# Kernel optimization log

Hardware: AMD Instinct MI355X
Metric: run time of the kernel (lower is better)

## Reference

```python
import jax, jax.numpy as jnp
import numpy as np

N_HEADS = 16
ROPE_BASE = 10000.0


def _rope_cos_sin(seq_len, head_dim, dtype):
    half = head_dim // 2
    inv_freq = 1.0 / (ROPE_BASE ** (jnp.arange(0, half, dtype=jnp.float32) / half))
    ang = jnp.arange(seq_len, dtype=jnp.float32)[:, None] * inv_freq[None, :]  # [S, half]
    cos = jnp.concatenate([jnp.cos(ang), jnp.cos(ang)], axis=-1).astype(dtype)  # [S, hd]
    sin = jnp.concatenate([jnp.sin(ang), jnp.sin(ang)], axis=-1).astype(dtype)
    return cos, sin


def _rotate_half(x):
    half = x.shape[-1] // 2
    return jnp.concatenate([-x[..., half:], x[..., :half]], axis=-1)


def setup_inputs() -> dict:
    key = jax.random.key(0)
    k1, k2, k3 = jax.random.split(key, 3)
    B, S, D = 2, 2048, 1024
    x = jax.random.normal(k1, (B, S, D), dtype=jnp.float32)
    w_qkv = jax.random.normal(k2, (D, 3 * D), dtype=jnp.float32) * (1.0 / np.sqrt(D))
    w_out = jax.random.normal(k3, (D, D), dtype=jnp.float32) * (1.0 / np.sqrt(D))
    return {"x": x, "w_qkv": w_qkv, "w_out": w_out}


def reference(x, w_qkv, w_out):
    B, S, D = x.shape
    H = N_HEADS
    hd = D // H
    scale = 1.0 / np.sqrt(hd)

    qkv = x @ w_qkv  # [B, S, 3D]
    q, k, v = jnp.split(qkv, 3, axis=-1)
    # [B, H, S, hd]
    q = q.reshape(B, S, H, hd).transpose(0, 2, 1, 3)
    k = k.reshape(B, S, H, hd).transpose(0, 2, 1, 3)
    v = v.reshape(B, S, H, hd).transpose(0, 2, 1, 3)

    cos, sin = _rope_cos_sin(S, hd, x.dtype)  # [S, hd]
    q = q * cos + _rotate_half(q) * sin
    k = k * cos + _rotate_half(k) * sin

    scores = jnp.einsum("bhqd,bhkd->bhqk", q, k) * scale  # [B, H, S, S]
    causal = jnp.tril(jnp.ones((S, S), dtype=bool))
    scores = jnp.where(causal[None, None, :, :], scores, -jnp.inf)

    probs = jax.nn.softmax(scores.astype(jnp.float32), axis=-1).astype(q.dtype)
    out = jnp.einsum("bhqk,bhkd->bhqd", probs, v)  # [B, H, S, hd]
    out = out.transpose(0, 2, 1, 3).reshape(B, S, D)
    return out @ w_out
```

## Files before the change

kernel.cpp:

```cpp
#include <hip/hip_runtime.h>
#include <math.h>
#include <type_traits>

#define B_  2
#define S_  2048
#define D_  1024
#define H_  16

typedef short bf16x8 __attribute__((ext_vector_type(8)));
typedef short bf16x4 __attribute__((ext_vector_type(4)));
typedef float f32x4  __attribute__((ext_vector_type(4)));

__device__ __forceinline__ short f2bf(float f) {
    unsigned u = __builtin_bit_cast(unsigned, f);
    u += 0x7FFFu + ((u >> 16) & 1u);
    return (short)(u >> 16);
}
__device__ __forceinline__ float bf2f(short s) {
    unsigned u = ((unsigned)(unsigned short)s) << 16;
    return __builtin_bit_cast(float, u);
}

__device__ __forceinline__ void gload16(const short* g, const void* l) {
    __builtin_amdgcn_global_load_lds(
        (const __attribute__((address_space(1))) void*)g,
        (__attribute__((address_space(3))) void*)l, 16, 0, 0);
}

__global__ __launch_bounds__(256) void cvt_bf16_kernel(
    const float* __restrict__ in, short* __restrict__ out)
{
    int i = (blockIdx.x * 256 + threadIdx.x) * 8;
    float4 a = *(const float4*)(in + i);
    float4 b = *(const float4*)(in + i + 4);
    bf16x8 o;
    o[0] = f2bf(a.x); o[1] = f2bf(a.y); o[2] = f2bf(a.z); o[3] = f2bf(a.w);
    o[4] = f2bf(b.x); o[5] = f2bf(b.y); o[6] = f2bf(b.z); o[7] = f2bf(b.w);
    *(bf16x8*)(out + i) = o;
}

__global__ __launch_bounds__(256) void transpose_cvt_kernel(
    const float* __restrict__ in, short* __restrict__ out, int K, int N)
{
    __shared__ short t[64][72];
    const int k0 = blockIdx.y * 64, n0 = blockIdx.x * 64;
    const int r = threadIdx.x >> 2;
    const int c = (threadIdx.x & 3) * 16;
    const float* src = in + (size_t)(k0 + r) * N + n0 + c;
#pragma unroll
    for (int i = 0; i < 16; ++i) t[c + i][r] = f2bf(src[i]);
    __syncthreads();
    short* dst = out + (size_t)(n0 + r) * K + k0 + c;
    *(bf16x8*)(dst)     = *(const bf16x8*)&t[r][c];
    *(bf16x8*)(dst + 8) = *(const bf16x8*)&t[r][c + 8];
}

__global__ __launch_bounds__(256) void rope_tab_kernel(float2* __restrict__ tab)
{
    int idx = blockIdx.x * 256 + threadIdx.x;
    int j = idx & 31, s = idx >> 5;
    float inv = powf(10000.0f, -(float)j * (1.0f / 32.0f));
    float sn, cs;
    sincosf((float)s * inv, &sn, &cs);
    tab[idx] = make_float2(cs, sn);
}

__global__ __launch_bounds__(256) void gemm_bt_f32(
    const short* __restrict__ A, const short* __restrict__ Bt,
    float* __restrict__ C, int M, int N, int K)
{
    __shared__ short smem[18432];

    const int tid  = threadIdx.x;
    const int wave = tid >> 6, lane = tid & 63;
    const int quad = lane >> 4, l16 = lane & 15;
    const int wm = wave >> 1, wn = wave & 1;
    const int row0 = blockIdx.y * 128, col0 = blockIdx.x * 64;

    f32x4 acc[4][2];
#pragma unroll
    for (int mi = 0; mi < 4; ++mi)
#pragma unroll
        for (int ni = 0; ni < 2; ++ni) acc[mi][ni] = (f32x4)0.f;

    const int sr = tid >> 2;
    const int sc = (tid & 3) * 8;
    const short* a0 = A  + (size_t)(row0 + sr) * K + sc;
    const short* a1 = A  + (size_t)(row0 + 64 + sr) * K + sc;
    const short* b0 = Bt + (size_t)(col0 + sr) * K + sc;

    auto stage = [&](int b, int kt) {
        char* l = (char*)(smem + b * 6144) + wave * 1024;
        const int k0 = kt * 32;
        gload16(a0 + k0, l);
        gload16(a1 + k0, l + 4096);
        gload16(b0 + k0, l + 8192);
    };

    const int NT = K >> 5;
    stage(0, 0);
    stage(1, 1);
    int bufid = 0;
    for (int kt = 0; kt < NT; ++kt) {
        if (kt + 1 < NT) { asm volatile("s_waitcnt vmcnt(3)" ::: "memory"); }
        else             { asm volatile("s_waitcnt vmcnt(0)" ::: "memory"); }
        __builtin_amdgcn_s_barrier();
        __builtin_amdgcn_sched_barrier(0);
        if (kt + 2 < NT) {
            int nb = bufid + 2; if (nb >= 3) nb -= 3;
            stage(nb, kt + 2);
        }

        const short* As = smem + bufid * 6144;
        const short* Bs = As + 4096;
        bf16x8 af[4], bfr[2];
#pragma unroll
        for (int mi = 0; mi < 4; ++mi)
            af[mi] = *(const bf16x8*)(As + (wm * 64 + mi * 16 + l16) * 32 + quad * 8);
#pragma unroll
        for (int ni = 0; ni < 2; ++ni)
            bfr[ni] = *(const bf16x8*)(Bs + (wn * 32 + ni * 16 + l16) * 32 + quad * 8);
#pragma unroll
        for (int mi = 0; mi < 4; ++mi)
#pragma unroll
            for (int ni = 0; ni < 2; ++ni)
                acc[mi][ni] = __builtin_amdgcn_mfma_f32_16x16x32_bf16(
                    af[mi], bfr[ni], acc[mi][ni], 0, 0, 0);

        bufid = (bufid + 1 == 3) ? 0 : bufid + 1;
    }

#pragma unroll
    for (int mi = 0; mi < 4; ++mi)
#pragma unroll
        for (int ni = 0; ni < 2; ++ni)
#pragma unroll
            for (int r = 0; r < 4; ++r) {
                int row = row0 + wm * 64 + mi * 16 + quad * 4 + r;
                int col = col0 + wn * 32 + ni * 16 + l16;
                C[(size_t)row * N + col] = acc[mi][ni][r];
            }
}

__global__ __launch_bounds__(256) void gemm_qkv(
    const short* __restrict__ A, const short* __restrict__ Bt,
    const float2* __restrict__ tab,
    short* __restrict__ Qb, short* __restrict__ Kb, short* __restrict__ Vt)
{
    const int K = 1024;
    extern __shared__ short smem[];
    short* Sc = smem;

    const int tid  = threadIdx.x;
    const int wave = tid >> 6, lane = tid & 63;
    const int quad = lane >> 4, l16 = lane & 15;
    const int wm = wave >> 1, wn = wave & 1;
    const int row0 = blockIdx.y * 128, col0 = blockIdx.x * 128;

    f32x4 acc[4][4];
#pragma unroll
    for (int mi = 0; mi < 4; ++mi)
#pragma unroll
        for (int ni = 0; ni < 4; ++ni) acc[mi][ni] = (f32x4)0.f;

    const int sr = tid >> 2;
    const int sc = (tid & 3) * 8;
    const short* a0 = A  + (size_t)(row0 + sr) * K + sc;
    const short* a1 = A  + (size_t)(row0 + 64 + sr) * K + sc;
    const short* b0 = Bt + (size_t)(col0 + sr) * K + sc;
    const short* b1 = Bt + (size_t)(col0 + 64 + sr) * K + sc;

    auto stage = [&](int b, int kt) {
        char* l = (char*)(smem + b * 8192) + wave * 1024;
        const int k0 = kt * 32;
        gload16(a0 + k0, l);
        gload16(a1 + k0, l + 4096);
        gload16(b0 + k0, l + 8192);
        gload16(b1 + k0, l + 12288);
    };

    const int NT = K >> 5;
    stage(0, 0);
    stage(1, 1);
    int bufid = 0;
    for (int kt = 0; kt < NT; ++kt) {
        if (kt + 1 < NT) { asm volatile("s_waitcnt vmcnt(4)" ::: "memory"); }
        else             { asm volatile("s_waitcnt vmcnt(0)" ::: "memory"); }
        __builtin_amdgcn_s_barrier();
        __builtin_amdgcn_sched_barrier(0);
        if (kt + 2 < NT) {
            int nb = bufid + 2; if (nb >= 3) nb -= 3;
            stage(nb, kt + 2);
        }

        const short* As = smem + bufid * 8192;
        const short* Bs = As + 4096;
        bf16x8 af[4], bfr[4];
#pragma unroll
        for (int mi = 0; mi < 4; ++mi)
            af[mi] = *(const bf16x8*)(As + (wm * 64 + mi * 16 + l16) * 32 + quad * 8);
#pragma unroll
        for (int ni = 0; ni < 4; ++ni)
            bfr[ni] = *(const bf16x8*)(Bs + (wn * 64 + ni * 16 + l16) * 32 + quad * 8);
#pragma unroll
        for (int mi = 0; mi < 4; ++mi)
#pragma unroll
            for (int ni = 0; ni < 4; ++ni)
                acc[mi][ni] = __builtin_amdgcn_mfma_f32_16x16x32_bf16(
                    af[mi], bfr[ni], acc[mi][ni], 0, 0, 0);

        bufid = (bufid + 1 == 3) ? 0 : bufid + 1;
    }

    __syncthreads();

    const int sec  = (col0 + wn * 64) >> 6;
    const int h    = sec & 15;
    const int kind = sec >> 4;
    short* myS = Sc + wave * 4608;

    const int mrow0 = row0 + wm * 64;
    const int b  = mrow0 >> 11;
    const int bh = b * 16 + h;
    const int sbase = mrow0 & (S_ - 1);

    if (kind < 2) {
#pragma unroll
        for (int mi = 0; mi < 4; ++mi) {
#pragma unroll
            for (int r = 0; r < 4; ++r) {
                int sl = mi * 16 + quad * 4 + r;
                int s = sbase + sl;
#pragma unroll
                for (int ni = 0; ni < 2; ++ni) {
                    int j = ni * 16 + l16;
                    float2 t = tab[s * 32 + j];
                    float lo = acc[mi][ni][r], hi = acc[mi][ni + 2][r];
                    float olo = lo * t.x - hi * t.y;
                    float ohi = hi * t.x + lo * t.y;
                    if (kind == 0) { olo *= 0.125f; ohi *= 0.125f; }
                    myS[sl * 72 + j]      = f2bf(olo);
                    myS[sl * 72 + 32 + j] = f2bf(ohi);
                }
            }
        }
        const int rl = lane >> 3;
        const int cl = (lane & 7) * 8;
        short* dst = (kind == 0 ? Qb : Kb);
#pragma unroll
        for (int p = 0; p < 8; ++p) {
            int rr = p * 8 + rl;
            bf16x8 v = *(const bf16x8*)&myS[rr * 72 + cl];
            *(bf16x8*)(dst + ((size_t)bh * S_ + sbase + rr) * 64 + cl) = v;
        }
    } else {
#pragma unroll
        for (int mi = 0; mi < 4; ++mi)
#pragma unroll
            for (int ni = 0; ni < 4; ++ni) {
                bf16x4 p;
                p[0] = f2bf(acc[mi][ni][0]);
                p[1] = f2bf(acc[mi][ni][1]);
                p[2] = f2bf(acc[mi][ni][2]);
                p[3] = f2bf(acc[mi][ni][3]);
                *(bf16x4*)&myS[(ni * 16 + l16) * 72 + mi * 16 + quad * 4] = p;
            }
        const int rl = lane >> 3;
        const int cl = (lane & 7) * 8;
#pragma unroll
        for (int p = 0; p < 8; ++p) {
            int dd = p * 8 + rl;
            bf16x8 v = *(const bf16x8*)&myS[dd * 72 + cl];
            *(bf16x8*)(Vt + ((size_t)bh * 64 + dd) * S_ + sbase + cl) = v;
        }
    }
}

__global__ __launch_bounds__(256, 3) void attn_kernel(
    const short* __restrict__ Qb, const short* __restrict__ Kb,
    const short* __restrict__ Vt, short* __restrict__ Opart,
    float* __restrict__ lpart)
{
    __shared__ short Ks[2][64 * 64];
    __shared__ short Vs[2][64 * 64];
    __shared__ short Ps[128][72];

    const int lin = blockIdx.x;
    const int xcd = lin & 7;
    const int j   = lin >> 3;
    const int bh   = xcd * 4 + (j & 3);
    const int task = j >> 2;

    const int g = task < 4 ? 0 : task < 12 ? 1 : task < 24 ? 2 : 3;
    const int cumstart = g == 0 ? 0 : g == 1 ? 4 : g == 2 ? 12 : 24;
    const int idx = task - cumstart;
    const int qd = idx / (g + 1);
    const int qb = 4 * g + qd;
    const int c  = idx - qd * (g + 1);
    const int t0 = c * 8;
    const int t1 = min(2 * qb + 1, c * 8 + 7);

    const int wave = threadIdx.x >> 6, lane = threadIdx.x & 63;
    const int quad = lane >> 4, l16 = lane & 15;
    const int subr  = lane >> 3;
    const int chunk = (lane & 7) ^ subr;
    const size_t head64 = (size_t)bh * S_ * 64;

    bf16x8 qf[2][2];
#pragma unroll
    for (int m = 0; m < 2; ++m) {
        const short* qrow = Qb + head64
            + (size_t)(qb * 128 + wave * 32 + m * 16 + l16) * 64 + quad * 8;
        qf[m][0] = *(const bf16x8*)(qrow);
        qf[m][1] = *(const bf16x8*)(qrow + 32);
    }

    bf16x8 ones;
#pragma unroll
    for (int i = 0; i < 8; ++i) ones[i] = (short)0x3F80;

    auto stage = [&](int buf, int t) {
        const short* kt = Kb + head64 + (size_t)(t * 64 + wave * 16) * 64;
        const short* vt = Vt + head64 + (size_t)(wave * 16) * S_ + t * 64;
        char* kl = (char*)(Ks[buf]) + wave * 2048;
        char* vl = (char*)(Vs[buf]) + wave * 2048;
#pragma unroll
        for (int g2 = 0; g2 < 2; ++g2) {
            gload16(kt + (g2 * 8 + subr) * 64 + chunk * 8, kl + g2 * 1024);
            gload16(vt + (size_t)(g2 * 8 + subr) * S_ + chunk * 8, vl + g2 * 1024);
        }
    };

    f32x4 lacc[2] = {(f32x4)0.f, (f32x4)0.f};
    f32x4 oacc[2][4];
#pragma unroll
    for (int m = 0; m < 2; ++m)
#pragma unroll
        for (int nt = 0; nt < 4; ++nt) oacc[m][nt] = (f32x4)0.f;

    stage(0, t0);
    int buf = 0;
    for (int t = t0; t <= t1; ++t) {
        __builtin_amdgcn_s_barrier();
        if (t < t1) stage(buf ^ 1, t + 1);
        if (t < t1) { asm volatile("s_waitcnt vmcnt(4)" ::: "memory"); }
        else        { asm volatile("s_waitcnt vmcnt(0)" ::: "memory"); }
        __builtin_amdgcn_s_barrier();
        __builtin_amdgcn_sched_barrier(0);

        const short* kbuf = Ks[buf];
        const short* vbuf = Vs[buf];

        f32x4 s4[2][4];
#pragma unroll
        for (int nt = 0; nt < 4; ++nt) {
            const int krow = nt * 16 + l16;
            const int sw = krow & 7;
            bf16x8 k0 = *(const bf16x8*)(kbuf + krow * 64 + ((quad ^ sw) << 3));
            bf16x8 k1 = *(const bf16x8*)(kbuf + krow * 64 + (((quad + 4) ^ sw) << 3));
#pragma unroll
            for (int m = 0; m < 2; ++m) {
                f32x4 a = (f32x4)0.f;
                a = __builtin_amdgcn_mfma_f32_16x16x32_bf16(k0, qf[m][0], a, 0, 0, 0);
                a = __builtin_amdgcn_mfma_f32_16x16x32_bf16(k1, qf[m][1], a, 0, 0, 0);
                s4[m][nt] = a;
            }
        }

        if (t >= 2 * qb) {
            const int kbase = (t - 2 * qb) * 64;
#pragma unroll
            for (int m = 0; m < 2; ++m) {
                const int qq = wave * 32 + m * 16 + l16;
#pragma unroll
                for (int nt = 0; nt < 4; ++nt)
#pragma unroll
                    for (int r = 0; r < 4; ++r)
                        if (kbase + nt * 16 + quad * 4 + r > qq)
                            s4[m][nt][r] = -INFINITY;
            }
        }

#pragma unroll
        for (int m = 0; m < 2; ++m)
#pragma unroll
            for (int nt = 0; nt < 4; ++nt) {
                bf16x4 p;
#pragma unroll
                for (int r = 0; r < 4; ++r)
                    p[r] = f2bf(__expf(s4[m][nt][r] - 8.0f));
                *(bf16x4*)&Ps[wave * 32 + m * 16 + l16][nt * 16 + quad * 4] = p;
            }

        bf16x8 pa[2][2];
#pragma unroll
        for (int m = 0; m < 2; ++m) {
            pa[m][0] = *(const bf16x8*)&Ps[wave * 32 + m * 16 + l16][quad * 8];
            pa[m][1] = *(const bf16x8*)&Ps[wave * 32 + m * 16 + l16][32 + quad * 8];
        }

#pragma unroll
        for (int m = 0; m < 2; ++m) {
            lacc[m] = __builtin_amdgcn_mfma_f32_16x16x32_bf16(pa[m][0], ones, lacc[m], 0, 0, 0);
            lacc[m] = __builtin_amdgcn_mfma_f32_16x16x32_bf16(pa[m][1], ones, lacc[m], 0, 0, 0);
        }

#pragma unroll
        for (int nt = 0; nt < 4; ++nt) {
            const int vrow = nt * 16 + l16;
            const int sw = vrow & 7;
            bf16x8 v0 = *(const bf16x8*)(vbuf + vrow * 64 + ((quad ^ sw) << 3));
            bf16x8 v1 = *(const bf16x8*)(vbuf + vrow * 64 + (((quad + 4) ^ sw) << 3));
#pragma unroll
            for (int m = 0; m < 2; ++m) {
                oacc[m][nt] = __builtin_amdgcn_mfma_f32_16x16x32_bf16(
                    pa[m][0], v0, oacc[m][nt], 0, 0, 0);
                oacc[m][nt] = __builtin_amdgcn_mfma_f32_16x16x32_bf16(
                    pa[m][1], v1, oacc[m][nt], 0, 0, 0);
            }
        }
        buf ^= 1;
    }

    const int pidx = bh * 40 + task;
#pragma unroll
    for (int m = 0; m < 2; ++m)
#pragma unroll
        for (int r = 0; r < 4; ++r) {
            int ql = wave * 32 + m * 16 + quad * 4 + r;
            short* orow = Opart + (size_t)pidx * 8192 + ql * 64;
#pragma unroll
            for (int nt = 0; nt < 4; ++nt)
                orow[nt * 16 + l16] = f2bf(oacc[m][nt][r]);
            if (l16 == 0)
                lpart[(size_t)pidx * 128 + ql] = lacc[m][r];
        }
}

__global__ __launch_bounds__(256) void combine_kernel(
    const short* __restrict__ Opart, const float* __restrict__ lpart,
    short* __restrict__ attnb)
{
    const int qb = blockIdx.x, bh = blockIdx.y;
    const int g = qb >> 2, nch = g + 1;
    const int cumstart = g == 0 ? 0 : g == 1 ? 4 : g == 2 ? 12 : 24;
    const int cbase = bh * 40 + cumstart + (qb - 4 * g) * nch;
    const int q = threadIdx.x >> 1;
    const int dg = (threadIdx.x & 1) * 32;

    float lsum = 0.f;
    float acc[32];
#pragma unroll
    for (int i = 0; i < 32; ++i) acc[i] = 0.f;

    for (int cc = 0; cc < nch; ++cc) {
        lsum += lpart[(size_t)(cbase + cc) * 128 + q];
        const short* src = Opart + (size_t)(cbase + cc) * 8192 + q * 64 + dg;
#pragma unroll
        for (int w = 0; w < 4; ++w) {
            bf16x8 o = *(const bf16x8*)(src + w * 8);
#pragma unroll
            for (int i = 0; i < 8; ++i) acc[w * 8 + i] += bf2f(o[i]);
        }
    }
    float inv = 1.0f / lsum;
    const int b = bh >> 4, h = bh & 15;
    short* dst = attnb + (size_t)(b * S_ + qb * 128 + q) * 1024 + h * 64 + dg;
#pragma unroll
    for (int w = 0; w < 4; ++w) {
        bf16x8 r;
#pragma unroll
        for (int i = 0; i < 8; ++i) r[i] = f2bf(acc[w * 8 + i] * inv);
        *(bf16x8*)(dst + w * 8) = r;
    }
}

extern "C" void kernel_launch(void* const* d_in, const int* in_sizes, int n_in,
                              void* d_out, int out_size, void* d_ws, size_t ws_size,
                              hipStream_t stream)
{
    const float* x     = (const float*)d_in[0];
    const float* w_qkv = (const float*)d_in[1];
    const float* w_out = (const float*)d_in[2];
    float* out = (float*)d_out;

    short* Qb   = (short*)d_ws;
    short* Kb   = Qb   + (size_t)4096 * 1024;
    short* Vt   = Kb   + (size_t)4096 * 1024;
    short* Xb   = Vt   + (size_t)4096 * 1024;
    short* Wqt  = Xb   + (size_t)4096 * 1024;
    short* Wot  = Wqt  + (size_t)3072 * 1024;
    float2* tab = (float2*)(Wot + (size_t)1024 * 1024);
    short* Opart = (short*)(tab + 2048 * 32);
    float* lbuf  = (float*)(Opart + (size_t)1280 * 8192);
    short* attnb = Xb;

    cvt_bf16_kernel<<<(4096 * 1024 / 8) / 256, 256, 0, stream>>>(x, Xb);
    transpose_cvt_kernel<<<dim3(3072 / 64, 1024 / 64), 256, 0, stream>>>(
        w_qkv, Wqt, 1024, 3072);
    transpose_cvt_kernel<<<dim3(1024 / 64, 1024 / 64), 256, 0, stream>>>(
        w_out, Wot, 1024, 1024);
    rope_tab_kernel<<<(2048 * 32) / 256, 256, 0, stream>>>(tab);

    gemm_qkv<<<dim3(3072 / 128, 4096 / 128), 256, 49152, stream>>>(
        Xb, Wqt, tab, Qb, Kb, Vt);

    attn_kernel<<<1280, 256, 0, stream>>>(Qb, Kb, Vt, Opart, lbuf);

    combine_kernel<<<dim3(16, 32), 256, 0, stream>>>(Opart, lbuf, attnb);

    gemm_bt_f32<<<dim3(1024 / 64, 4096 / 128), 256, 0, stream>>>(
        attnb, Wot, out, 4096, 1024, 1024);
}
```

Measured before the change: 178.5 us.

## Fuse prep kernels, swizzle GEMM block order for XCDs, add MFMA priority hints

```diff
diff --git a/kernel.cpp b/kernel.cpp
--- a/kernel.cpp
+++ b/kernel.cpp
@@ -27,25 +27,13 @@
         (__attribute__((address_space(3))) void*)l, 16, 0, 0);
 }
 
-__global__ __launch_bounds__(256) void cvt_bf16_kernel(
-    const float* __restrict__ in, short* __restrict__ out)
-{
-    int i = (blockIdx.x * 256 + threadIdx.x) * 8;
-    float4 a = *(const float4*)(in + i);
-    float4 b = *(const float4*)(in + i + 4);
-    bf16x8 o;
-    o[0] = f2bf(a.x); o[1] = f2bf(a.y); o[2] = f2bf(a.z); o[3] = f2bf(a.w);
-    o[4] = f2bf(b.x); o[5] = f2bf(b.y); o[6] = f2bf(b.z); o[7] = f2bf(b.w);
-    *(bf16x8*)(out + i) = o;
-}
-
-__global__ __launch_bounds__(256) void transpose_cvt_kernel(
-    const float* __restrict__ in, short* __restrict__ out, int K, int N)
-{
-    __shared__ short t[64][72];
-    const int k0 = blockIdx.y * 64, n0 = blockIdx.x * 64;
-    const int r = threadIdx.x >> 2;
-    const int c = (threadIdx.x & 3) * 16;
+__device__ __forceinline__ void transpose_body(
+    const float* __restrict__ in, short* __restrict__ out, int K, int N,
+    int bx, int by, short (*t)[72], int tid)
+{
+    const int k0 = by * 64, n0 = bx * 64;
+    const int r = tid >> 2;
+    const int c = (tid & 3) * 16;
     const float* src = in + (size_t)(k0 + r) * N + n0 + c;
 #pragma unroll
     for (int i = 0; i < 16; ++i) t[c + i][r] = f2bf(src[i]);
@@ -55,14 +43,37 @@
     *(bf16x8*)(dst + 8) = *(const bf16x8*)&t[r][c + 8];
 }
 
-__global__ __launch_bounds__(256) void rope_tab_kernel(float2* __restrict__ tab)
-{
-    int idx = blockIdx.x * 256 + threadIdx.x;
-    int j = idx & 31, s = idx >> 5;
-    float inv = powf(10000.0f, -(float)j * (1.0f / 32.0f));
-    float sn, cs;
-    sincosf((float)s * inv, &sn, &cs);
-    tab[idx] = make_float2(cs, sn);
+__global__ __launch_bounds__(256) void prep_kernel(
+    const float* __restrict__ x, short* __restrict__ Xb,
+    const float* __restrict__ w_qkv, short* __restrict__ Wqt,
+    const float* __restrict__ w_out, short* __restrict__ Wot,
+    float2* __restrict__ tab)
+{
+    __shared__ short t[64][72];
+    const int bid = blockIdx.x;
+    const int tid = threadIdx.x;
+    if (bid < 2048) {
+        int i = (bid * 256 + tid) * 8;
+        float4 a = *(const float4*)(x + i);
+        float4 b = *(const float4*)(x + i + 4);
+        bf16x8 o;
+        o[0] = f2bf(a.x); o[1] = f2bf(a.y); o[2] = f2bf(a.z); o[3] = f2bf(a.w);
+        o[4] = f2bf(b.x); o[5] = f2bf(b.y); o[6] = f2bf(b.z); o[7] = f2bf(b.w);
+        *(bf16x8*)(Xb + i) = o;
+    } else if (bid < 2816) {
+        int b2 = bid - 2048;
+        transpose_body(w_qkv, Wqt, 1024, 3072, b2 % 48, b2 / 48, t, tid);
+    } else if (bid < 3072) {
+        int b2 = bid - 2816;
+        transpose_body(w_out, Wot, 1024, 1024, b2 % 16, b2 / 16, t, tid);
+    } else {
+        int idx = (bid - 3072) * 256 + tid;
+        int j = idx & 31, s = idx >> 5;
+        float inv = powf(10000.0f, -(float)j * (1.0f / 32.0f));
+        float sn, cs;
+        sincosf((float)s * inv, &sn, &cs);
+        tab[idx] = make_float2(cs, sn);
+    }
 }
 
 __global__ __launch_bounds__(256) void gemm_bt_f32(
@@ -75,7 +86,12 @@
     const int wave = tid >> 6, lane = tid & 63;
     const int quad = lane >> 4, l16 = lane & 15;
     const int wm = wave >> 1, wn = wave & 1;
-    const int row0 = blockIdx.y * 128, col0 = blockIdx.x * 64;
+
+    const int nbx = N >> 6;
+    const int cpx = gridDim.x >> 3;
+    const int lin = blockIdx.x;
+    const int swz = (lin & 7) * cpx + (lin >> 3);
+    const int row0 = (swz / nbx) * 128, col0 = (swz % nbx) * 64;
 
     f32x4 acc[4][2];
 #pragma unroll
@@ -155,7 +171,10 @@
     const int wave = tid >> 6, lane = tid & 63;
     const int quad = lane >> 4, l16 = lane & 15;
     const int wm = wave >> 1, wn = wave & 1;
-    const int row0 = blockIdx.y * 128, col0 = blockIdx.x * 128;
+
+    const int lin = blockIdx.x;
+    const int swz = (lin & 7) * 96 + (lin >> 3);
+    const int row0 = (swz / 24) * 128, col0 = (swz % 24) * 128;
 
     f32x4 acc[4][4];
 #pragma unroll
@@ -352,6 +371,7 @@
         const short* vbuf = Vs[buf];
 
         f32x4 s4[2][4];
+        __builtin_amdgcn_s_setprio(1);
 #pragma unroll
         for (int nt = 0; nt < 4; ++nt) {
             const int krow = nt * 16 + l16;
@@ -366,6 +386,7 @@
                 s4[m][nt] = a;
             }
         }
+        __builtin_amdgcn_s_setprio(0);
 
         if (t >= 2 * qb) {
             const int kbase = (t - 2 * qb) * 64;
@@ -399,12 +420,12 @@
             pa[m][1] = *(const bf16x8*)&Ps[wave * 32 + m * 16 + l16][32 + quad * 8];
         }
 
+        __builtin_amdgcn_s_setprio(1);
 #pragma unroll
         for (int m = 0; m < 2; ++m) {
             lacc[m] = __builtin_amdgcn_mfma_f32_16x16x32_bf16(pa[m][0], ones, lacc[m], 0, 0, 0);
             lacc[m] = __builtin_amdgcn_mfma_f32_16x16x32_bf16(pa[m][1], ones, lacc[m], 0, 0, 0);
         }
-
 #pragma unroll
         for (int nt = 0; nt < 4; ++nt) {
             const int vrow = nt * 16 + l16;
@@ -419,6 +440,7 @@
                     pa[m][1], v1, oacc[m][nt], 0, 0, 0);
             }
         }
+        __builtin_amdgcn_s_setprio(0);
         buf ^= 1;
     }
 
@@ -495,20 +517,13 @@
     float* lbuf  = (float*)(Opart + (size_t)1280 * 8192);
     short* attnb = Xb;
 
-    cvt_bf16_kernel<<<(4096 * 1024 / 8) / 256, 256, 0, stream>>>(x, Xb);
-    transpose_cvt_kernel<<<dim3(3072 / 64, 1024 / 64), 256, 0, stream>>>(
-        w_qkv, Wqt, 1024, 3072);
-    transpose_cvt_kernel<<<dim3(1024 / 64, 1024 / 64), 256, 0, stream>>>(
-        w_out, Wot, 1024, 1024);
-    rope_tab_kernel<<<(2048 * 32) / 256, 256, 0, stream>>>(tab);
-
-    gemm_qkv<<<dim3(3072 / 128, 4096 / 128), 256, 49152, stream>>>(
-        Xb, Wqt, tab, Qb, Kb, Vt);
+    prep_kernel<<<3328, 256, 0, stream>>>(x, Xb, w_qkv, Wqt, w_out, Wot, tab);
+
+    gemm_qkv<<<768, 256, 49152, stream>>>(Xb, Wqt, tab, Qb, Kb, Vt);
 
     attn_kernel<<<1280, 256, 0, stream>>>(Qb, Kb, Vt, Opart, lbuf);
 
     combine_kernel<<<dim3(16, 32), 256, 0, stream>>>(Opart, lbuf, attnb);
 
-    gemm_bt_f32<<<dim3(1024 / 64, 4096 / 128), 256, 0, stream>>>(
-        attnb, Wot, out, 4096, 1024, 1024);
-}
+    gemm_bt_f32<<<512, 256, 0, stream>>>(attnb, Wot, out, 4096, 1024, 1024);
+}
```

Measured after the change: 175.6 us (median of 2 runs). About the same (-1.6%).
